# Kernel optimization log

Hardware: AMD Instinct MI355X
Metric: run time of the kernel (lower is better)

## Reference

```python
import jax, jax.numpy as jnp
import numpy as np

# TISA RBF basis (helpers l2_dist / rbf_basis in the repo): f_i(d) = a_i * exp(-|b_i| * (d - c_i)^2)

def setup_inputs() -> dict:
    key = jax.random.key(0)
    k = jax.random.split(key, 8)
    B, L, H, D, S, F = 2, 2048, 8, 64, 2, 5
    qs = jax.random.normal(k[0], (B, L, H, D), dtype=jnp.float32)
    ks = jax.random.normal(k[1], (B, L, H, D), dtype=jnp.float32)
    vs = jax.random.normal(k[2], (B, L, H, D), dtype=jnp.float32)
    qs_s = jax.random.uniform(k[3], (B, L, S), dtype=jnp.float32)
    ks_s = jax.random.uniform(k[4], (B, L, S), dtype=jnp.float32)
    a = jax.random.uniform(k[5], (H * F,), dtype=jnp.float32)
    b = jax.random.uniform(k[6], (H * F,), dtype=jnp.float32)
    c = jax.random.normal(k[7], (H * F,), dtype=jnp.float32) * 0.5
    return {"qs": qs, "ks": ks, "vs": vs, "qs_s": qs_s, "ks_s": ks_s, "a": a, "b": b, "c": c}


def _tisa_attention(qs, ks, vs, qs_s, ks_s, a, b, c):
    B, Q, H, D = qs.shape
    F = a.size // H
    aH, bH, cH = (p.reshape(H, F) for p in (a, b, c))
    # pairwise euclidean distance between query and key locations: [B, Q, K]
    diff = qs_s[:, :, None, :] - ks_s[:, None, :, :]
    d = jnp.sqrt(jnp.sum(diff * diff, axis=-1))
    d_ = d[:, None]  # [B, 1, Q, K] broadcast over heads
    # RBF bias summed over F basis functions (small fixed F -> python sum avoids B,H,F,Q,K blowup)
    bias = sum(
        aH[:, f][None, :, None, None]
        * jnp.exp(-jnp.abs(bH[:, f])[None, :, None, None] * (d_ - cH[:, f][None, :, None, None]) ** 2)
        for f in range(F)
    )  # [B, H, Q, K]
    scale = 1.0 / jnp.sqrt(jnp.asarray(D, dtype=qs.dtype))
    scores = jnp.einsum('bqhd,bkhd->bhqk', qs * scale, ks) + bias
    attn = jax.nn.softmax(scores, axis=-1)
    return jnp.einsum('bhqk,bkhd->bqhd', attn, vs)


def reference(qs, ks, vs, qs_s, ks_s, a, b, c):
    # Matches scan_tisa_biased_attention: online-softmax chunking is mathematically
    # identical to a single stable softmax over the full key axis.
    return _tisa_attention(qs, ks, vs, qs_s, ks_s, a, b, c)
```

## Files before the change

### kernel.cpp

```cpp
#include <hip/hip_runtime.h>
#include <cmath>

typedef _Float16 half8 __attribute__((ext_vector_type(8)));
typedef _Float16 half4 __attribute__((ext_vector_type(4)));
typedef _Float16 half2v __attribute__((ext_vector_type(2)));
typedef float f32x4 __attribute__((ext_vector_type(4)));
typedef float f32x2 __attribute__((ext_vector_type(2)));

#define B_ 2
#define L_ 2048
#define H_ 8
#define D_ 64
#define S_ 2
#define F_ 5
#define LUTN 2048
#define LSCALE 1448.1547f
#define LOG2E 1.44269504f
#define QSC (0.125f * LOG2E)

#define QOFF 0
#define KOFF 2097152
#define VOFF 4194304
#define SOFFH 6291456
#define WS_NEED 12615680

#define OFF_K 0
#define OFF_V 16384
#define OFF_LUT 32768
#define ARENA_SZ 40976
#define SLOTF (16 * 68 + 16)

#define GLOBAL_LOAD_LDS16(g, l)                                                  \
  __builtin_amdgcn_global_load_lds((const __attribute__((address_space(1))) void*)(g), \
                                   (__attribute__((address_space(3))) void*)(l), 16, 0, 0)

#define FAST_SQRT(x) __builtin_amdgcn_sqrtf(x)

__global__ __launch_bounds__(256, 4)
void tisa_preproc(const float* __restrict__ qs, const float* __restrict__ ks,
                  const float* __restrict__ vs, const float* __restrict__ ks_s,
                  _Float16* __restrict__ wsh) {
  __shared__ _Float16 Vl[64 * 72];
  const int t = threadIdx.x;
  const int u = blockIdx.x & 31;
  const int bh = blockIdx.x >> 5;
  const size_t base = ((size_t)(bh >> 3) * L_ + (size_t)u * 64) * (H_ * D_) + (size_t)(bh & 7) * D_;

#pragma unroll
  for (int jj = 0; jj < 2; ++jj) {
    int id = t * 2 + jj;
    int row = id >> 3, c = id & 7;
    const float* src = qs + base + (size_t)row * 512 + c * 8;
    f32x4 x0 = ((const f32x4*)src)[0], x1 = ((const f32x4*)src)[1];
    half8 hh;
#pragma unroll
    for (int k = 0; k < 4; ++k) { hh[k] = (_Float16)(x0[k] * QSC); hh[k + 4] = (_Float16)(x1[k] * QSC); }
    *(half8*)&wsh[QOFF + ((size_t)bh * 32 + u) * 4096 + row * 64 + (c ^ (row & 7)) * 8] = hh;
  }
#pragma unroll
  for (int jj = 0; jj < 2; ++jj) {
    int id = t * 2 + jj;
    int tile = id >> 8, row = (id >> 3) & 31, c = id & 7;
    const float* src = ks + base + (size_t)(tile * 32 + row) * 512 + c * 8;
    f32x4 x0 = ((const f32x4*)src)[0], x1 = ((const f32x4*)src)[1];
    half8 hh;
#pragma unroll
    for (int k = 0; k < 4; ++k) { hh[k] = (_Float16)x0[k]; hh[k + 4] = (_Float16)x1[k]; }
    *(half8*)&wsh[KOFF + ((size_t)bh * 64 + u * 2 + tile) * 2048 + row * 64 + (c ^ (row & 7)) * 8] = hh;
  }
  if ((bh & 7) == 0 && t < 32) {
    const int b = bh >> 3;
    const float* src = ks_s + ((size_t)b * L_ + u * 64) * 2 + t * 4;
    float* dst = (float*)(wsh + SOFFH) + ((size_t)b * L_ + u * 64) * 2 + t * 4;
    f32x4 x = *(const f32x4*)src;
    x *= LSCALE;
    *(f32x4*)dst = x;
  }
  {
    int key = t >> 2, d0 = (t & 3) * 16;
    const float* src = vs + base + (size_t)key * 512 + d0;
    f32x4 a0 = ((const f32x4*)src)[0], a1 = ((const f32x4*)src)[1];
    f32x4 a2 = ((const f32x4*)src)[2], a3 = ((const f32x4*)src)[3];
    half8 h0, h1;
#pragma unroll
    for (int k = 0; k < 4; ++k) {
      h0[k] = (_Float16)a0[k]; h0[k + 4] = (_Float16)a1[k];
      h1[k] = (_Float16)a2[k]; h1[k + 4] = (_Float16)a3[k];
    }
    *(half8*)&Vl[key * 72 + d0] = h0;
    *(half8*)&Vl[key * 72 + d0 + 8] = h1;
  }
  __syncthreads();
#pragma unroll
  for (int jj = 0; jj < 2; ++jj) {
    int id = t * 2 + jj;
    int tile = id >> 8, s = (id >> 3) & 31, cp2 = id & 7;
    int d = 2 * s + (cp2 >> 2), kb = (cp2 & 3) * 8;
    half8 hh;
#pragma unroll
    for (int j = 0; j < 8; ++j) {
      int kpj = kb + j;
      int orig = ((kpj >> 2) & 1) * 16 + (kpj >> 3) * 4 + (kpj & 3);
      hh[j] = Vl[(tile * 32 + orig) * 72 + d];
    }
    *(half8*)&wsh[VOFF + ((size_t)bh * 64 + u * 2 + tile) * 2048 + s * 64 + (cp2 ^ (s & 7)) * 8] = hh;
  }
}

__global__ __launch_bounds__(1024, 8)
void tisa_attn_main(const float* __restrict__ qs_s, const float* __restrict__ ap,
                    const float* __restrict__ bp, const float* __restrict__ cp,
                    const _Float16* __restrict__ wsh, float* __restrict__ out) {
  __shared__ __align__(16) char arena[ARENA_SZ];
  float* LUT = (float*)(arena + OFF_LUT);

  const int t = threadIdx.x;
  const int lane = t & 63;
  const int w = t >> 6;
  const int g = w >> 2;
  const int qw = w & 3;
  const int t2 = t & 255;
  const int quad = lane >> 4;
  const int l16 = lane & 15;

  const int qt = blockIdx.x & 31;
  const int bh = blockIdx.x >> 5;
  const int h = bh & 7;
  const int b = bh >> 3;
  const int q0 = qt * 64;

  {
    float af[F_], nb[F_], cf[F_];
#pragma unroll
    for (int f = 0; f < F_; ++f) {
      af[f] = ap[h * F_ + f];
      nb[f] = -fabsf(bp[h * F_ + f]);
      cf[f] = cp[h * F_ + f];
    }
    for (int i = t; i <= LUTN; i += 1024) {
      float d = ((float)i + 0.5f) * (1.0f / LSCALE);
      float s = 0.f;
#pragma unroll
      for (int f = 0; f < F_; ++f) {
        float e = d - cf[f];
        s += af[f] * __expf(nb[f] * (e * e));
      }
      LUT[i] = (s - 8.0f) * LOG2E;
    }
  }

  const float qx = qs_s[((size_t)b * L_ + q0 + qw * 16 + l16) * 2 + 0] * LSCALE;
  const float qy = qs_s[((size_t)b * L_ + q0 + qw * 16 + l16) * 2 + 1] * LSCALE;

  const _Float16* Qt = wsh + QOFF + ((size_t)bh * 32 + qt) * 4096;
  const _Float16* Kbh = wsh + KOFF + (size_t)bh * 64 * 2048;
  const _Float16* Vbh = wsh + VOFF + (size_t)bh * 64 * 2048;
  const float* wsS = (const float*)(wsh + SOFFH);

  if (w < 8)
    GLOBAL_LOAD_LDS16(Qt + w * 512 + lane * 8, arena + OFF_K + w * 1024);
  __syncthreads();

  half8 qA[2];
#pragma unroll
  for (int kb = 0; kb < 2; ++kb)
    qA[kb] = *(const half8*)(arena + OFF_K + (qw * 16 + l16) * 128 +
                             ((kb * 4 + quad) ^ (l16 & 7)) * 16);

  f32x4 oc[4];
#pragma unroll
  for (int df = 0; df < 4; ++df) oc[df] = (f32x4){0.f, 0.f, 0.f, 0.f};
  f32x4 lsacc = (f32x4){0.f, 0.f, 0.f, 0.f};
  half8 onesv;
#pragma unroll
  for (int j = 0; j < 8; ++j) onesv[j] = (_Float16)1.0f;

  const _Float16* ksrc = Kbh + (size_t)(g * 16) * 2048 + t2 * 8;
  const _Float16* vsrc = Vbh + (size_t)(g * 16) * 2048 + t2 * 8;
  const float* sbase = wsS + ((size_t)b * L_ + g * 512 + quad * 4) * 2;
  char* kdst = arena + OFF_K + g * 4096 + qw * 1024;
  char* vdst = arena + OFF_V + g * 4096 + qw * 1024;

  for (int it = 0; it < 16; ++it) {
    __syncthreads();
    GLOBAL_LOAD_LDS16(ksrc, kdst);
    GLOBAL_LOAD_LDS16(vsrc, vdst);
    ksrc += 2048; vsrc += 2048;
    __syncthreads();

    const float* sit = sbase + it * 64;
    f32x4 c01a = *(const f32x4*)(sit);
    f32x4 c23a = *(const f32x4*)(sit + 4);
    f32x4 c01b = *(const f32x4*)(sit + 32);
    f32x4 c23b = *(const f32x4*)(sit + 36);

    f32x4 acc[2];
#pragma unroll
    for (int nf = 0; nf < 2; ++nf) {
      f32x4 a = (f32x4){0.f, 0.f, 0.f, 0.f};
#pragma unroll
      for (int kb = 0; kb < 2; ++kb) {
        half8 kf = *(const half8*)(arena + OFF_K + g * 4096 + (nf * 16 + l16) * 128 +
                                   ((kb * 4 + quad) ^ (l16 & 7)) * 16);
        a = __builtin_amdgcn_mfma_f32_16x16x32_f16(kf, qA[kb], a, 0, 0, 0);
      }
      acc[nf] = a;
    }

    half8 pw;
#pragma unroll
    for (int nf = 0; nf < 2; ++nf) {
      f32x4 cA = (nf == 0) ? c01a : c01b;
      f32x4 cB = (nf == 0) ? c23a : c23b;
      float kxr[4] = {cA.x, cA.z, cB.x, cB.z};
      float kyr[4] = {cA.y, cA.w, cB.y, cB.w};
#pragma unroll
      for (int r = 0; r < 4; ++r) {
        float dx = qx - kxr[r], dy = qy - kyr[r];
        float tt = FAST_SQRT(fmaf(dx, dx, dy * dy));
        int ii = (int)tt;
        float p = __builtin_amdgcn_exp2f(acc[nf][r] + LUT[ii]);
        pw[nf * 4 + r] = (_Float16)p;
      }
    }

    lsacc = __builtin_amdgcn_mfma_f32_16x16x32_f16(pw, onesv, lsacc, 0, 0, 0);
#pragma unroll
    for (int df = 0; df < 4; ++df) {
      half8 vf = *(const half8*)(arena + OFF_V + g * 4096 + (l16 >> 1) * 128 + df * 1024 +
                                 ((((l16 & 1) * 4 + quad) ^ ((l16 >> 1) & 7)) * 16));
      oc[df] = __builtin_amdgcn_mfma_f32_16x16x32_f16(pw, vf, oc[df], 0, 0, 0);
    }
  }

  float lred[4];
#pragma unroll
  for (int r = 0; r < 4; ++r) lred[r] = lsacc[r];
  __syncthreads();
  float* slots = (float*)arena;
  if (g >= 2) {
    float* sl = slots + ((g - 2) * 4 + qw) * SLOTF;
#pragma unroll
    for (int df = 0; df < 4; ++df)
#pragma unroll
      for (int r = 0; r < 4; ++r)
        sl[(quad * 4 + r) * 68 + df * 16 + l16] = oc[df][r];
    if (l16 == 0) {
#pragma unroll
      for (int r = 0; r < 4; ++r) sl[16 * 68 + quad * 4 + r] = lred[r];
    }
  }
  __syncthreads();
  if (g < 2) {
    float* sl = slots + (g * 4 + qw) * SLOTF;
#pragma unroll
    for (int df = 0; df < 4; ++df)
#pragma unroll
      for (int r = 0; r < 4; ++r)
        oc[df][r] += sl[(quad * 4 + r) * 68 + df * 16 + l16];
#pragma unroll
    for (int r = 0; r < 4; ++r) lred[r] += sl[16 * 68 + quad * 4 + r];
  }
  if (g == 1) {
    float* sl = slots + (4 + qw) * SLOTF;
#pragma unroll
    for (int df = 0; df < 4; ++df)
#pragma unroll
      for (int r = 0; r < 4; ++r)
        sl[(quad * 4 + r) * 68 + df * 16 + l16] = oc[df][r];
    if (l16 == 0) {
#pragma unroll
      for (int r = 0; r < 4; ++r) sl[16 * 68 + quad * 4 + r] = lred[r];
    }
  }
  __syncthreads();
  if (g == 0) {
    float* sl = slots + (4 + qw) * SLOTF;
    float inv_l[4];
#pragma unroll
    for (int r = 0; r < 4; ++r)
      inv_l[r] = 1.f / (lred[r] + sl[16 * 68 + quad * 4 + r]);
#pragma unroll
    for (int df = 0; df < 4; ++df)
#pragma unroll
      for (int r = 0; r < 4; ++r) {
        int qrow = q0 + qw * 16 + quad * 4 + r;
        float v = oc[df][r] + sl[(quad * 4 + r) * 68 + df * 16 + l16];
        out[((size_t)(b * L_ + qrow)) * (H_ * D_) + h * D_ + df * 16 + l16] = v * inv_l[r];
      }
  }
}

#define KSTR 72
#define PH 72
#define FLUTN 512
#define FLSCALE 362.03867f
__global__ __launch_bounds__(512, 4)
void tisa_attn_fallback(const float* __restrict__ qs, const float* __restrict__ ks,
                        const float* __restrict__ vs, const float* __restrict__ qs_s,
                        const float* __restrict__ ks_s, const float* __restrict__ ap,
                        const float* __restrict__ bp, const float* __restrict__ cp,
                        float* __restrict__ out) {
  __shared__ _Float16 Ks[2][64 * KSTR];
  __shared__ _Float16 VT[2][D_ * KSTR];
  __shared__ _Float16 Pf[8][16 * PH];
  __shared__ float kss2[2][64 * 2];
  __shared__ f32x2 LUT2s[FLUTN + 1];
  __shared__ float comb[4][16][64];
  __shared__ float combl[4][16];

  const int t = threadIdx.x;
  const int lane = t & 63;
  const int w = t >> 6;
  const int g = w >> 2;
  const int qw = w & 3;
  const int t2 = t & 255;
  const int quad = lane >> 4;
  const int l16 = lane & 15;
  const int qt = blockIdx.x & 31;
  const int bh = blockIdx.x >> 5;
  const int h = bh & 7;
  const int b = bh >> 3;
  const int q0 = qt * 64;

  float af[F_], nb[F_], cf[F_];
#pragma unroll
  for (int f = 0; f < F_; ++f) {
    af[f] = ap[h * F_ + f];
    nb[f] = -fabsf(bp[h * F_ + f]);
    cf[f] = cp[h * F_ + f];
  }
  for (int i = t; i <= FLUTN; i += 512) {
    float d0 = (float)i * (1.0f / FLSCALE), d1 = (float)(i + 1) * (1.0f / FLSCALE);
    float s0 = 0.f, s1 = 0.f;
#pragma unroll
    for (int f = 0; f < F_; ++f) {
      float e0 = d0 - cf[f], e1 = d1 - cf[f];
      s0 += af[f] * __expf(nb[f] * (e0 * e0));
      s1 += af[f] * __expf(nb[f] * (e1 * e1));
    }
    LUT2s[i] = (f32x2){s0 - 8.0f, s1 - 8.0f};
  }
  float qx[4], qy[4];
#pragma unroll
  for (int r = 0; r < 4; ++r) {
    int qrow = q0 + qw * 16 + quad * 4 + r;
    qx[r] = qs_s[(b * L_ + qrow) * S_ + 0];
    qy[r] = qs_s[(b * L_ + qrow) * S_ + 1];
  }
  if (t < 256) {
    const int row = t >> 2, dc = (t & 3) * 16;
    const float* src = qs + (((size_t)(b * L_ + q0 + row)) * H_ + h) * D_ + dc;
    const f32x4* s4 = (const f32x4*)src;
    f32x4 v0 = s4[0], v1 = s4[1], v2 = s4[2], v3 = s4[3];
    half8 w0, w1;
#pragma unroll
    for (int u = 0; u < 4; ++u) {
      w0[u] = (_Float16)(v0[u] * 0.125f); w0[u + 4] = (_Float16)(v1[u] * 0.125f);
      w1[u] = (_Float16)(v2[u] * 0.125f); w1[u + 4] = (_Float16)(v3[u] * 0.125f);
    }
    *(half8*)&Ks[0][row * KSTR + dc] = w0;
    *(half8*)&Ks[0][row * KSTR + dc + 8] = w1;
  }
  __syncthreads();
  half8 qA[2];
#pragma unroll
  for (int kb = 0; kb < 2; ++kb)
    qA[kb] = *(const half8*)&Ks[0][(qw * 16 + l16) * KSTR + kb * 32 + quad * 8];
  f32x4 oc[4];
#pragma unroll
  for (int df = 0; df < 4; ++df) oc[df] = (f32x4){0.f, 0.f, 0.f, 0.f};
  float l_r[4] = {0.f, 0.f, 0.f, 0.f};

  for (int it = 0; it < 16; ++it) {
    const int k0 = (g * 16 + it) * 64;
    __syncthreads();
    {
      const int row = t2 >> 2, dc = (t2 & 3) * 16;
      const float* src = ks + (((size_t)(b * L_ + k0 + row)) * H_ + h) * D_ + dc;
      const f32x4* s4 = (const f32x4*)src;
      f32x4 v0 = s4[0], v1 = s4[1], v2 = s4[2], v3 = s4[3];
      half8 w0, w1;
#pragma unroll
      for (int u = 0; u < 4; ++u) {
        w0[u] = (_Float16)v0[u]; w0[u + 4] = (_Float16)v1[u];
        w1[u] = (_Float16)v2[u]; w1[u + 4] = (_Float16)v3[u];
      }
      *(half8*)&Ks[g][row * KSTR + dc] = w0;
      *(half8*)&Ks[g][row * KSTR + dc + 8] = w1;
    }
    {
      const int kk = (t2 & 31) * 2, dg = (t2 >> 5) * 8;
      const float* s0 = vs + (((size_t)(b * L_ + k0 + kk)) * H_ + h) * D_ + dg;
      const float* s1 = s0 + H_ * D_;
      f32x4 a0 = ((const f32x4*)s0)[0], a1 = ((const f32x4*)s0)[1];
      f32x4 b0 = ((const f32x4*)s1)[0], b1 = ((const f32x4*)s1)[1];
#pragma unroll
      for (int u = 0; u < 4; ++u) {
        half2v p0 = {(_Float16)a0[u], (_Float16)b0[u]};
        *(half2v*)&VT[g][(dg + u) * KSTR + kk] = p0;
        half2v p1 = {(_Float16)a1[u], (_Float16)b1[u]};
        *(half2v*)&VT[g][(dg + 4 + u) * KSTR + kk] = p1;
      }
    }
    if (t2 < 128) kss2[g][t2] = ks_s[((size_t)(b * L_) + k0 + (t2 >> 1)) * S_ + (t2 & 1)];
    __syncthreads();
    f32x4 acc[4];
#pragma unroll
    for (int nf = 0; nf < 4; ++nf) {
      f32x4 a = (f32x4){0.f, 0.f, 0.f, 0.f};
#pragma unroll
      for (int kb = 0; kb < 2; ++kb) {
        half8 kf = *(const half8*)&Ks[g][(nf * 16 + l16) * KSTR + kb * 32 + quad * 8];
        a = __builtin_amdgcn_mfma_f32_16x16x32_f16(qA[kb], kf, a, 0, 0, 0);
      }
      acc[nf] = a;
    }
#pragma unroll
    for (int nf = 0; nf < 4; ++nf) {
      float kx = kss2[g][(nf * 16 + l16) * 2 + 0];
      float ky = kss2[g][(nf * 16 + l16) * 2 + 1];
#pragma unroll
      for (int r = 0; r < 4; ++r) {
        float dx = qx[r] - kx, dy = qy[r] - ky;
        float dist = FAST_SQRT(fmaf(dx, dx, dy * dy));
        float tt = dist * FLSCALE;
        int ii = (int)tt;
        float fr = tt - (float)ii;
        f32x2 lh = LUT2s[ii];
        float p = __expf(acc[nf][r] + fmaf(fr, lh.y - lh.x, lh.x));
        acc[nf][r] = p;
      }
    }
#pragma unroll
    for (int r = 0; r < 4; ++r)
      l_r[r] += (acc[0][r] + acc[1][r]) + (acc[2][r] + acc[3][r]);
#pragma unroll
    for (int nf = 0; nf < 4; ++nf)
#pragma unroll
      for (int r = 0; r < 4; ++r)
        Pf[w][(quad * 4 + r) * PH + nf * 16 + l16] = (_Float16)acc[nf][r];
#pragma unroll
    for (int kb = 0; kb < 2; ++kb) {
      half8 pa = *(const half8*)&Pf[w][l16 * PH + kb * 32 + quad * 8];
#pragma unroll
      for (int df = 0; df < 4; ++df) {
        half8 vf = *(const half8*)&VT[g][(df * 16 + l16) * KSTR + kb * 32 + quad * 8];
        oc[df] = __builtin_amdgcn_mfma_f32_16x16x32_f16(pa, vf, oc[df], 0, 0, 0);
      }
    }
  }
  __syncthreads();
  float lred[4];
#pragma unroll
  for (int r = 0; r < 4; ++r) {
    float s = l_r[r];
    s += __shfl_xor(s, 1); s += __shfl_xor(s, 2);
    s += __shfl_xor(s, 4); s += __shfl_xor(s, 8);
    lred[r] = s;
  }
  if (g == 1) {
#pragma unroll
    for (int df = 0; df < 4; ++df)
#pragma unroll
      for (int r = 0; r < 4; ++r)
        comb[qw][quad * 4 + r][df * 16 + l16] = oc[df][r];
    if (l16 == 0) {
#pragma unroll
      for (int r = 0; r < 4; ++r) combl[qw][quad * 4 + r] = lred[r];
    }
  }
  __syncthreads();
  if (g == 0) {
    float inv_l[4];
#pragma unroll
    for (int r = 0; r < 4; ++r)
      inv_l[r] = 1.f / (lred[r] + combl[qw][quad * 4 + r]);
#pragma unroll
    for (int df = 0; df < 4; ++df)
#pragma unroll
      for (int r = 0; r < 4; ++r) {
        int qrow = q0 + qw * 16 + quad * 4 + r;
        float v = oc[df][r] + combl[qw][quad * 4 + r] * 0.f + comb[qw][quad * 4 + r][df * 16 + l16];
        out[(((size_t)(b * L_ + qrow)) * H_ + h) * D_ + df * 16 + l16] = v * inv_l[r];
      }
  }
}

extern "C" void kernel_launch(void* const* d_in, const int* in_sizes, int n_in,
                              void* d_out, int out_size, void* d_ws, size_t ws_size,
                              hipStream_t stream) {
  const float* qs = (const float*)d_in[0];
  const float* ks = (const float*)d_in[1];
  const float* vs = (const float*)d_in[2];
  const float* qs_s = (const float*)d_in[3];
  const float* ks_s = (const float*)d_in[4];
  const float* ap = (const float*)d_in[5];
  const float* bp = (const float*)d_in[6];
  const float* cp = (const float*)d_in[7];
  float* out = (float*)d_out;

  if (ws_size >= (size_t)WS_NEED) {
    _Float16* wsh = (_Float16*)d_ws;
    tisa_preproc<<<dim3(512), dim3(256), 0, stream>>>(qs, ks, vs, ks_s, wsh);
    tisa_attn_main<<<dim3(512), dim3(1024), 0, stream>>>(qs_s, ap, bp, cp, wsh, out);
  } else {
    tisa_attn_fallback<<<dim3(512), dim3(512), 0, stream>>>(qs, ks, vs, qs_s, ks_s, ap, bp, cp, out);
  }
}
```

Measured before the change: 133.9 us.

## Double-buffer K/V tiles, remap blocks per XCD, widen preproc blocks, pack fp16 converts

After: 129.4 us. 1.04x faster.

```diff
diff --git a/kernel.cpp b/kernel.cpp
--- a/kernel.cpp
+++ b/kernel.cpp
@@ -4,6 +4,7 @@
 typedef _Float16 half8 __attribute__((ext_vector_type(8)));
 typedef _Float16 half4 __attribute__((ext_vector_type(4)));
 typedef _Float16 half2v __attribute__((ext_vector_type(2)));
+typedef __fp16 fp16x2 __attribute__((ext_vector_type(2)));
 typedef float f32x4 __attribute__((ext_vector_type(4)));
 typedef float f32x2 __attribute__((ext_vector_type(2)));
 
@@ -24,10 +25,12 @@
 #define SOFFH 6291456
 #define WS_NEED 12615680
 
-#define OFF_K 0
-#define OFF_V 16384
-#define OFF_LUT 32768
-#define ARENA_SZ 40976
+#define OFF_K0 0
+#define OFF_K1 16384
+#define OFF_V0 32768
+#define OFF_V1 49152
+#define OFF_LUT 65536
+#define ARENA_SZ 73744
 #define SLOTF (16 * 68 + 16)
 
 #define GLOBAL_LOAD_LDS16(g, l)                                                  \
@@ -36,20 +39,20 @@
 
 #define FAST_SQRT(x) __builtin_amdgcn_sqrtf(x)
 
-__global__ __launch_bounds__(256, 4)
+__global__ __launch_bounds__(512, 4)
 void tisa_preproc(const float* __restrict__ qs, const float* __restrict__ ks,
                   const float* __restrict__ vs, const float* __restrict__ ks_s,
                   _Float16* __restrict__ wsh) {
   __shared__ _Float16 Vl[64 * 72];
   const int t = threadIdx.x;
-  const int u = blockIdx.x & 31;
-  const int bh = blockIdx.x >> 5;
+  const int bid = blockIdx.x;
+  const int xcd = bid & 7, slot = bid >> 3;
+  const int u = slot & 31;
+  const int bh = xcd * 2 + (slot >> 5);
   const size_t base = ((size_t)(bh >> 3) * L_ + (size_t)u * 64) * (H_ * D_) + (size_t)(bh & 7) * D_;
 
-#pragma unroll
-  for (int jj = 0; jj < 2; ++jj) {
-    int id = t * 2 + jj;
-    int row = id >> 3, c = id & 7;
+  {
+    int row = t >> 3, c = t & 7;
     const float* src = qs + base + (size_t)row * 512 + c * 8;
     f32x4 x0 = ((const f32x4*)src)[0], x1 = ((const f32x4*)src)[1];
     half8 hh;
@@ -57,10 +60,8 @@
     for (int k = 0; k < 4; ++k) { hh[k] = (_Float16)(x0[k] * QSC); hh[k + 4] = (_Float16)(x1[k] * QSC); }
     *(half8*)&wsh[QOFF + ((size_t)bh * 32 + u) * 4096 + row * 64 + (c ^ (row & 7)) * 8] = hh;
   }
-#pragma unroll
-  for (int jj = 0; jj < 2; ++jj) {
-    int id = t * 2 + jj;
-    int tile = id >> 8, row = (id >> 3) & 31, c = id & 7;
+  {
+    int tile = t >> 8, row = (t >> 3) & 31, c = t & 7;
     const float* src = ks + base + (size_t)(tile * 32 + row) * 512 + c * 8;
     f32x4 x0 = ((const f32x4*)src)[0], x1 = ((const f32x4*)src)[1];
     half8 hh;
@@ -77,24 +78,17 @@
     *(f32x4*)dst = x;
   }
   {
-    int key = t >> 2, d0 = (t & 3) * 16;
-    const float* src = vs + base + (size_t)key * 512 + d0;
+    int key = t >> 3, seg = t & 7;
+    const float* src = vs + base + (size_t)key * 512 + seg * 8;
     f32x4 a0 = ((const f32x4*)src)[0], a1 = ((const f32x4*)src)[1];
-    f32x4 a2 = ((const f32x4*)src)[2], a3 = ((const f32x4*)src)[3];
-    half8 h0, h1;
-#pragma unroll
-    for (int k = 0; k < 4; ++k) {
-      h0[k] = (_Float16)a0[k]; h0[k + 4] = (_Float16)a1[k];
-      h1[k] = (_Float16)a2[k]; h1[k + 4] = (_Float16)a3[k];
-    }
-    *(half8*)&Vl[key * 72 + d0] = h0;
-    *(half8*)&Vl[key * 72 + d0 + 8] = h1;
-  }
-  __syncthreads();
-#pragma unroll
-  for (int jj = 0; jj < 2; ++jj) {
-    int id = t * 2 + jj;
-    int tile = id >> 8, s = (id >> 3) & 31, cp2 = id & 7;
+    half8 h0;
+#pragma unroll
+    for (int k = 0; k < 4; ++k) { h0[k] = (_Float16)a0[k]; h0[k + 4] = (_Float16)a1[k]; }
+    *(half8*)&Vl[key * 72 + seg * 8] = h0;
+  }
+  __syncthreads();
+  {
+    int tile = t >> 8, s = (t >> 3) & 31, cp2 = t & 7;
     int d = 2 * s + (cp2 >> 2), kb = (cp2 & 3) * 8;
     half8 hh;
 #pragma unroll
@@ -123,8 +117,10 @@
   const int quad = lane >> 4;
   const int l16 = lane & 15;
 
-  const int qt = blockIdx.x & 31;
-  const int bh = blockIdx.x >> 5;
+  const int bid = blockIdx.x;
+  const int xcd = bid & 7, slot = bid >> 3;
+  const int qt = slot & 31;
+  const int bh = xcd * 2 + (slot >> 5);
   const int h = bh & 7;
   const int b = bh >> 3;
   const int q0 = qt * 64;
@@ -157,15 +153,23 @@
   const _Float16* Vbh = wsh + VOFF + (size_t)bh * 64 * 2048;
   const float* wsS = (const float*)(wsh + SOFFH);
 
+  const _Float16* ksrc = Kbh + (size_t)(g * 16) * 2048 + t2 * 8;
+  const _Float16* vsrc = Vbh + (size_t)(g * 16) * 2048 + t2 * 8;
+  const float* sbase = wsS + ((size_t)b * L_ + g * 512 + quad * 4) * 2;
+
   if (w < 8)
-    GLOBAL_LOAD_LDS16(Qt + w * 512 + lane * 8, arena + OFF_K + w * 1024);
+    GLOBAL_LOAD_LDS16(Qt + w * 512 + lane * 8, arena + OFF_K1 + w * 1024);
+  GLOBAL_LOAD_LDS16(ksrc, arena + OFF_K0 + g * 4096 + qw * 1024);
+  GLOBAL_LOAD_LDS16(vsrc, arena + OFF_V0 + g * 4096 + qw * 1024);
+  ksrc += 2048; vsrc += 2048;
   __syncthreads();
 
   half8 qA[2];
 #pragma unroll
   for (int kb = 0; kb < 2; ++kb)
-    qA[kb] = *(const half8*)(arena + OFF_K + (qw * 16 + l16) * 128 +
+    qA[kb] = *(const half8*)(arena + OFF_K1 + (qw * 16 + l16) * 128 +
                              ((kb * 4 + quad) ^ (l16 & 7)) * 16);
+  __syncthreads();
 
   f32x4 oc[4];
 #pragma unroll
@@ -175,18 +179,14 @@
 #pragma unroll
   for (int j = 0; j < 8; ++j) onesv[j] = (_Float16)1.0f;
 
-  const _Float16* ksrc = Kbh + (size_t)(g * 16) * 2048 + t2 * 8;
-  const _Float16* vsrc = Vbh + (size_t)(g * 16) * 2048 + t2 * 8;
-  const float* sbase = wsS + ((size_t)b * L_ + g * 512 + quad * 4) * 2;
-  char* kdst = arena + OFF_K + g * 4096 + qw * 1024;
-  char* vdst = arena + OFF_V + g * 4096 + qw * 1024;
-
+  int cur16 = 0;
   for (int it = 0; it < 16; ++it) {
-    __syncthreads();
-    GLOBAL_LOAD_LDS16(ksrc, kdst);
-    GLOBAL_LOAD_LDS16(vsrc, vdst);
-    ksrc += 2048; vsrc += 2048;
-    __syncthreads();
+    const int nxt16 = cur16 ^ 16384;
+    if (it < 15) {
+      GLOBAL_LOAD_LDS16(ksrc, arena + OFF_K0 + nxt16 + g * 4096 + qw * 1024);
+      GLOBAL_LOAD_LDS16(vsrc, arena + OFF_V0 + nxt16 + g * 4096 + qw * 1024);
+      ksrc += 2048; vsrc += 2048;
+    }
 
     const float* sit = sbase + it * 64;
     f32x4 c01a = *(const f32x4*)(sit);
@@ -200,14 +200,14 @@
       f32x4 a = (f32x4){0.f, 0.f, 0.f, 0.f};
 #pragma unroll
       for (int kb = 0; kb < 2; ++kb) {
-        half8 kf = *(const half8*)(arena + OFF_K + g * 4096 + (nf * 16 + l16) * 128 +
+        half8 kf = *(const half8*)(arena + OFF_K0 + cur16 + g * 4096 + (nf * 16 + l16) * 128 +
                                    ((kb * 4 + quad) ^ (l16 & 7)) * 16);
         a = __builtin_amdgcn_mfma_f32_16x16x32_f16(kf, qA[kb], a, 0, 0, 0);
       }
       acc[nf] = a;
     }
 
-    half8 pw;
+    float parr[8];
 #pragma unroll
     for (int nf = 0; nf < 2; ++nf) {
       f32x4 cA = (nf == 0) ? c01a : c01b;
@@ -219,18 +219,25 @@
         float dx = qx - kxr[r], dy = qy - kyr[r];
         float tt = FAST_SQRT(fmaf(dx, dx, dy * dy));
         int ii = (int)tt;
-        float p = __builtin_amdgcn_exp2f(acc[nf][r] + LUT[ii]);
-        pw[nf * 4 + r] = (_Float16)p;
-      }
-    }
+        parr[nf * 4 + r] = __builtin_amdgcn_exp2f(acc[nf][r] + LUT[ii]);
+      }
+    }
+    union { half8 h8; fp16x2 h2[4]; } pu;
+#pragma unroll
+    for (int k = 0; k < 4; ++k)
+      pu.h2[k] = __builtin_amdgcn_cvt_pkrtz(parr[2 * k], parr[2 * k + 1]);
+    half8 pw = pu.h8;
 
     lsacc = __builtin_amdgcn_mfma_f32_16x16x32_f16(pw, onesv, lsacc, 0, 0, 0);
 #pragma unroll
     for (int df = 0; df < 4; ++df) {
-      half8 vf = *(const half8*)(arena + OFF_V + g * 4096 + (l16 >> 1) * 128 + df * 1024 +
+      half8 vf = *(const half8*)(arena + OFF_V0 + cur16 + g * 4096 + (l16 >> 1) * 128 + df * 1024 +
                                  ((((l16 & 1) * 4 + quad) ^ ((l16 >> 1) & 7)) * 16));
       oc[df] = __builtin_amdgcn_mfma_f32_16x16x32_f16(pw, vf, oc[df], 0, 0, 0);
     }
+
+    __syncthreads();
+    cur16 = nxt16;
   }
 
   float lred[4];
@@ -502,7 +509,7 @@
 
   if (ws_size >= (size_t)WS_NEED) {
     _Float16* wsh = (_Float16*)d_ws;
-    tisa_preproc<<<dim3(512), dim3(256), 0, stream>>>(qs, ks, vs, ks_s, wsh);
+    tisa_preproc<<<dim3(512), dim3(512), 0, stream>>>(qs, ks, vs, ks_s, wsh);
     tisa_attn_main<<<dim3(512), dim3(1024), 0, stream>>>(qs_s, ap, bp, cp, wsh, out);
   } else {
     tisa_attn_fallback<<<dim3(512), dim3(512), 0, stream>>>(qs, ks, vs, qs_s, ks_s, ap, bp, cp, out);
```
